# Performance work log

Measured on AMD Instinct MI355X. Metric: run time of the kernel, lower is better.

## Reference

```python
import jax, jax.numpy as jnp
import numpy as np

B, LT, LE, D, H, M, BS = 4, 2048, 1024, 1024, 16, 4096, 128
HD = D // H            # head dim 64
NB = LT // BS          # 16 blocks
SINK_ITERS = 5
NEG = -1e9
SCALE = 1.0 / np.sqrt(HD).astype(np.float32)


def setup_inputs() -> dict:
    key = jax.random.key(0)
    ks = jax.random.split(key, 16)
    p = lambda k, shp: jax.random.normal(k, shp, jnp.float32) * 0.02
    return {
        "targets": jax.random.normal(ks[0], (B, LT, D), jnp.float32),
        "encoded": jax.random.normal(ks[1], (B, LE, D), jnp.float32),
        "ln1_s": jnp.ones((D,), jnp.float32), "ln1_b": jnp.zeros((D,), jnp.float32),
        "ln2_s": jnp.ones((D,), jnp.float32), "ln2_b": jnp.zeros((D,), jnp.float32),
        "ln3_s": jnp.ones((D,), jnp.float32), "ln3_b": jnp.zeros((D,), jnp.float32),
        "wq1": p(ks[2], (D, H, HD)), "wk1": p(ks[3], (D, H, HD)),
        "wv1": p(ks[4], (D, H, HD)), "wo1": p(ks[5], (H, HD, D)),
        "wsort": p(ks[6], (H, HD, NB)),
        "wq2": p(ks[7], (D, H, HD)), "wk2": p(ks[8], (D, H, HD)),
        "wv2": p(ks[9], (D, H, HD)), "wo2": p(ks[10], (H, HD, D)),
        "w1": p(ks[11], (D, M)), "b1": jnp.zeros((M,), jnp.float32),
        "w2": p(ks[12], (M, D)), "b2": jnp.zeros((D,), jnp.float32),
    }


def layer_norm(x, s, b, eps=1e-6):
    mu = jnp.mean(x, -1, keepdims=True)
    var = jnp.mean(jnp.square(x - mu), -1, keepdims=True)
    return (x - mu) * jax.lax.rsqrt(var + eps) * s + b


def causal_sinkhorn(logits):
    # logits: [B,H,NB,NB]. Causal block mask + iterative log-space row/col
    # normalization -> soft (doubly-stochastic-ish) block permutation matrix.
    mask = jnp.tril(jnp.ones((NB, NB), bool))
    la = jnp.where(mask, logits, NEG)
    for _ in range(SINK_ITERS):
        la = la - jax.nn.logsumexp(la, axis=-1, keepdims=True)
        la = jnp.where(mask, la, NEG)
        la = la - jax.nn.logsumexp(la, axis=-2, keepdims=True)
        la = jnp.where(mask, la, NEG)
    return jnp.exp(la)


def sinkhorn_self_attention(x, wq, wk, wv, wsort, wo):
    # x: [B,LT,D] -> blocked q/k/v: [B,NB,BS,H,HD]
    q = jnp.einsum('bld,dhk->blhk', x, wq).reshape(B, NB, BS, H, HD)
    k = jnp.einsum('bld,dhk->blhk', x, wk).reshape(B, NB, BS, H, HD)
    v = jnp.einsum('bld,dhk->blhk', x, wv).reshape(B, NB, BS, H, HD)
    # SortNet: sum-pooled block key representations -> block-to-block logits
    krep = jnp.sum(k, axis=2)                                   # [B,NB,H,HD]
    P = causal_sinkhorn(jnp.einsum('bnhk,hkm->bhnm', krep, wsort))  # [B,H,NB,NB]
    ks = jnp.einsum('bhij,bjshk->bishk', P, k)                  # sorted key blocks
    vs = jnp.einsum('bhij,bjshk->bishk', P, v)
    # each query block attends to (own block [causal]) ++ (sorted block)
    s_loc = jnp.einsum('bnqhk,bnshk->bhnqs', q, k) * SCALE      # [B,H,NB,BS,BS]
    s_srt = jnp.einsum('bnqhk,bnshk->bhnqs', q, ks) * SCALE
    cm = jnp.tril(jnp.ones((BS, BS), bool))
    s_loc = jnp.where(cm, s_loc, NEG)
    w = jax.nn.softmax(jnp.concatenate([s_loc, s_srt], axis=-1), axis=-1)
    o = (jnp.einsum('bhnqs,bnshk->bnqhk', w[..., :BS], v)
         + jnp.einsum('bhnqs,bnshk->bnqhk', w[..., BS:], vs))
    return jnp.einsum('blhk,hkd->bld', o.reshape(B, LT, H, HD), wo)


def cross_attention(x, kv, wq, wk, wv, wo):
    q = jnp.einsum('bld,dhk->blhk', x, wq)
    k = jnp.einsum('bld,dhk->blhk', kv, wk)
    v = jnp.einsum('bld,dhk->blhk', kv, wv)
    w = jax.nn.softmax(jnp.einsum('bqhk,bshk->bhqs', q, k) * SCALE, axis=-1)
    o = jnp.einsum('bhqs,bshk->bqhk', w, v)
    return jnp.einsum('blhk,hkd->bld', o, wo)


def reference(targets, encoded, ln1_s, ln1_b, ln2_s, ln2_b, ln3_s, ln3_b,
              wq1, wk1, wv1, wo1, wsort, wq2, wk2, wv2, wo2, w1, b1, w2, b2):
    x = layer_norm(targets, ln1_s, ln1_b)
    x = sinkhorn_self_attention(x, wq1, wk1, wv1, wsort, wo1) + targets
    y = layer_norm(x, ln2_s, ln2_b)
    y = cross_attention(y, encoded, wq2, wk2, wv2, wo2) + x
    z = layer_norm(y, ln3_s, ln3_b)
    z = jnp.dot(jax.nn.gelu(jnp.dot(z, w1) + b1), w2) + b2
    return y + z
```

## Files before the change

kernel.cpp:

```cpp
#include <hip/hip_runtime.h>

typedef unsigned short u16;
typedef __attribute__((ext_vector_type(8))) short short8;
typedef __attribute__((ext_vector_type(4))) short short4_t;
typedef __attribute__((ext_vector_type(4))) float float4_t;

#define B_ 4
#define LT_ 2048
#define LE_ 1024
#define D_ 1024
#define H_ 16
#define HD_ 64
#define NB_ 16
#define BS_ 128
#define M_ 4096
#define SCALE_ 0.125f

typedef __attribute__((address_space(1))) const void gas_t;
typedef __attribute__((address_space(3))) void las_t;

__device__ __forceinline__ float b2f(u16 u) {
  union { unsigned int i; float f; } v; v.i = ((unsigned int)u) << 16; return v.f;
}
__device__ __forceinline__ u16 f2b(float f) {
  union { float f; unsigned int i; } v; v.f = f;
  unsigned int x = v.i;
  return (u16)((x + 0x7fffu + ((x >> 16) & 1u)) >> 16);
}
__device__ __forceinline__ float gelu_f(float u) {
  float t = 0.7978845608028654f * (u + 0.044715f * u * u * u);
  float th = 1.f - 2.f / (__expf(2.f * t) + 1.f);
  return 0.5f * u * (1.f + th);
}
__device__ __forceinline__ void store_val(u16* p, float x) { *p = f2b(x); }
__device__ __forceinline__ void store_val(float* p, float x) { *p = x; }

__global__ __launch_bounds__(256)
void conv_k(const float* __restrict__ in, u16* __restrict__ out) {
  int i = (blockIdx.x * 256 + threadIdx.x) * 4;
  float4_t v = *(const float4_t*)(in + i);
  short4_t o;
  o[0] = (short)f2b(v[0]); o[1] = (short)f2b(v[1]);
  o[2] = (short)f2b(v[2]); o[3] = (short)f2b(v[3]);
  *(short4_t*)(out + i) = o;
}

__global__ __launch_bounds__(256)
void transpose_k(const float* __restrict__ in, u16* __restrict__ out, int R, int rstride) {
  __shared__ u16 tile[32][33];
  int bx = blockIdx.x * 32, by = blockIdx.y * 32;
  int tx = threadIdx.x & 31, ty = threadIdx.x >> 5;
  #pragma unroll
  for (int y = ty; y < 32; y += 8)
    tile[y][tx] = f2b(in[(size_t)(by + y) * rstride + bx + tx]);
  __syncthreads();
  #pragma unroll
  for (int y = ty; y < 32; y += 8)
    out[(size_t)(bx + y) * R + by + tx] = tile[tx][y];
}

#define NJOBS 10
struct TJobs {
  const float* src[NJOBS];
  u16* dst[NJOBS];
  int outR[NJOBS];
  int inS[NJOBS];
  int ntx[NJOBS];
  int ntiles[NJOBS];
};

__global__ __launch_bounds__(256)
void prep_k(TJobs J) {
  int t = blockIdx.x, j = 0;
  while (t >= J.ntiles[j]) { t -= J.ntiles[j]; ++j; }
  const float* in = J.src[j];
  u16* out = J.dst[j];
  const int R = J.outR[j], rstride = J.inS[j];
  const int bx = (t % J.ntx[j]) * 32, by = (t / J.ntx[j]) * 32;
  __shared__ u16 tile[32][33];
  int tx = threadIdx.x & 31, ty = threadIdx.x >> 5;
  #pragma unroll
  for (int y = ty; y < 32; y += 8)
    tile[y][tx] = f2b(in[(size_t)(by + y) * rstride + bx + tx]);
  __syncthreads();
  #pragma unroll
  for (int y = ty; y < 32; y += 8)
    out[(size_t)(bx + y) * R + by + tx] = tile[tx][y];
}

__global__ __launch_bounds__(256)
void ln_k(const float* __restrict__ x, const float* __restrict__ sw,
          const float* __restrict__ bw, u16* __restrict__ out) {
  int row = blockIdx.x, tid = threadIdx.x;
  const float* xr = x + (size_t)row * 1024 + tid * 4;
  float4_t raw = *(const float4_t*)xr;
  float v0 = raw[0], v1 = raw[1], v2 = raw[2], v3 = raw[3];
  float sum = v0 + v1 + v2 + v3;
  #pragma unroll
  for (int off = 32; off > 0; off >>= 1) sum += __shfl_down(sum, off, 64);
  __shared__ float sA[4], sB[4];
  int w = tid >> 6;
  if ((tid & 63) == 0) sA[w] = sum;
  __syncthreads();
  float mu = (sA[0] + sA[1] + sA[2] + sA[3]) * (1.f / 1024.f);
  float d0 = v0 - mu, d1 = v1 - mu, d2 = v2 - mu, d3 = v3 - mu;
  float s2 = d0 * d0 + d1 * d1 + d2 * d2 + d3 * d3;
  #pragma unroll
  for (int off = 32; off > 0; off >>= 1) s2 += __shfl_down(s2, off, 64);
  if ((tid & 63) == 0) sB[w] = s2;
  __syncthreads();
  float inv = rsqrtf((sB[0] + sB[1] + sB[2] + sB[3]) * (1.f / 1024.f) + 1e-6f);
  float4_t sv = *(const float4_t*)(sw + tid * 4);
  float4_t bv = *(const float4_t*)(bw + tid * 4);
  short4_t ov;
  ov[0] = (short)f2b(d0 * inv * sv[0] + bv[0]);
  ov[1] = (short)f2b(d1 * inv * sv[1] + bv[1]);
  ov[2] = (short)f2b(d2 * inv * sv[2] + bv[2]);
  ov[3] = (short)f2b(d3 * inv * sv[3] + bv[3]);
  *(short4_t*)(out + (size_t)row * 1024 + tid * 4) = ov;
}

template<int EPI, typename TC, int SPLIT>
__global__ __launch_bounds__(256)
void gemm_k(const u16* __restrict__ A, const u16* __restrict__ Bt,
            const float* __restrict__ bias, const float* __restrict__ res,
            TC* __restrict__ C, int M, int N, int K, size_t cstride) {
  __shared__ __align__(16) u16 lA[128 * 32];
  __shared__ __align__(16) u16 lB[128 * 32];
  const int gx = gridDim.x;
  int lin = blockIdx.y * gx + blockIdx.x;
  const int nwg = gx * gridDim.y;
  if (!(nwg & 7)) {
    const int chunk = nwg >> 3;
    lin = (lin & 7) * chunk + (lin >> 3);
  }
  const int bn = (lin % gx) * 128;
  const int bm = (lin / gx) * 128;
  const int tid = threadIdx.x;
  const int lane = tid & 63;
  const int wave = tid >> 6;
  const int wy = wave >> 1, wx = wave & 1;
  const int quad = lane >> 4, l16 = lane & 15;

  float4_t acc[4][4];
  float4_t zz = {0.f, 0.f, 0.f, 0.f};
  #pragma unroll
  for (int i = 0; i < 4; ++i)
    #pragma unroll
    for (int j = 0; j < 4; ++j) acc[i][j] = zz;

  const int r0 = tid >> 2, kc0 = (tid & 3) * 8;
  const u16* gA0 = A + (size_t)(bm + r0) * K + kc0;
  const u16* gA1 = A + (size_t)(bm + 64 + r0) * K + kc0;
  const u16* gB0 = Bt + (size_t)(bn + r0) * K + kc0;
  const u16* gB1 = Bt + (size_t)(bn + 64 + r0) * K + kc0;
  u16* lA0 = &lA[tid * 8];
  u16* lA1 = &lA[(tid + 256) * 8];
  u16* lB0 = &lB[tid * 8];
  u16* lB1 = &lB[(tid + 256) * 8];

  for (int k0 = 0; k0 < K; k0 += 32) {
    __syncthreads();
    __builtin_amdgcn_global_load_lds((gas_t*)(gA0 + k0), (las_t*)lA0, 16, 0, 0);
    __builtin_amdgcn_global_load_lds((gas_t*)(gA1 + k0), (las_t*)lA1, 16, 0, 0);
    __builtin_amdgcn_global_load_lds((gas_t*)(gB0 + k0), (las_t*)lB0, 16, 0, 0);
    __builtin_amdgcn_global_load_lds((gas_t*)(gB1 + k0), (las_t*)lB1, 16, 0, 0);
    __syncthreads();
    short8 af[4], bfr[4];
    #pragma unroll
    for (int i = 0; i < 4; ++i)
      af[i] = *(const short8*)&lA[(wy * 64 + i * 16 + l16) * 32 + quad * 8];
    #pragma unroll
    for (int j = 0; j < 4; ++j)
      bfr[j] = *(const short8*)&lB[(wx * 64 + j * 16 + l16) * 32 + quad * 8];
    #pragma unroll
    for (int i = 0; i < 4; ++i)
      #pragma unroll
      for (int j = 0; j < 4; ++j)
        acc[i][j] = __builtin_amdgcn_mfma_f32_16x16x32_bf16(af[i], bfr[j], acc[i][j], 0, 0, 0);
  }

  #pragma unroll
  for (int i = 0; i < 4; ++i) {
    int row = bm + wy * 64 + i * 16 + quad * 4;
    #pragma unroll
    for (int j = 0; j < 4; ++j) {
      int col = bn + wx * 64 + j * 16 + l16;
      TC* Cb = SPLIT ? (C + (size_t)(col >> 10) * cstride) : C;
      int ccol = SPLIT ? (col & 1023) : col;
      int cn = SPLIT ? 1024 : N;
      #pragma unroll
      for (int v = 0; v < 4; ++v) {
        float x = acc[i][j][v];
        size_t idx = (size_t)(row + v) * cn + ccol;
        if (EPI == 1) {
          x += res[idx];
        } else if (EPI == 2) {
          x = gelu_f(x + bias[col]);
        } else if (EPI == 3) {
          x += bias[col] + res[idx];
        }
        store_val(&Cb[idx], x);
      }
    }
  }
}

template<int EPI, typename TC, int SPLIT>
__global__ __launch_bounds__(512, 2)
void gemm256_k(const u16* __restrict__ A, const u16* __restrict__ Bt,
               const float* __restrict__ bias, const float* __restrict__ res,
               TC* __restrict__ C, int M, int N, int K, size_t cstride) {
  __shared__ __align__(16) u16 lA[4][256 * 32];
  __shared__ __align__(16) u16 lB[4][256 * 32];
  const int gx = gridDim.x;
  int lin = blockIdx.y * gx + blockIdx.x;
  const int nwg = gx * gridDim.y;
  if (!(nwg & 7)) {
    const int chunk = nwg >> 3;
    lin = (lin & 7) * chunk + (lin >> 3);
  }
  const int bn = (lin % gx) * 256;
  const int bm = (lin / gx) * 256;
  const int tid = threadIdx.x;
  const int lane = tid & 63;
  const int wave = tid >> 6;
  const int wy = wave >> 2, wx = wave & 3;
  const int quad = lane >> 4, l16 = lane & 15;
  const int slo = ((quad ^ ((l16 >> 1) & 3)) << 4);

  int lrow[2], kcs[2];
  #pragma unroll
  for (int u = 0; u < 2; ++u) {
    int p = (tid + u * 512) * 16;
    int lg = p ^ (((p >> 7) & 3) << 4);
    lrow[u] = lg >> 6;
    kcs[u] = (lg & 63) >> 1;
  }
  const u16* gA[2]; const u16* gB[2];
  #pragma unroll
  for (int u = 0; u < 2; ++u) {
    gA[u] = A + (size_t)(bm + lrow[u]) * K + kcs[u];
    gB[u] = Bt + (size_t)(bn + lrow[u]) * K + kcs[u];
  }
  const int NT = K >> 5;

  float4_t acc[8][4];
  float4_t zz = {0.f, 0.f, 0.f, 0.f};
  #pragma unroll
  for (int i = 0; i < 8; ++i)
    #pragma unroll
    for (int j = 0; j < 4; ++j) acc[i][j] = zz;

  #define STAGE256(TT, BUF)                                                      \
    {                                                                            \
      int kk_ = (TT) * 32;                                                       \
      __builtin_amdgcn_global_load_lds((gas_t*)(gA[0] + kk_),                    \
          (las_t*)((char*)&lA[BUF][0] + tid * 16), 16, 0, 0);                    \
      __builtin_amdgcn_global_load_lds((gas_t*)(gA[1] + kk_),                    \
          (las_t*)((char*)&lA[BUF][0] + (tid + 512) * 16), 16, 0, 0);            \
      __builtin_amdgcn_global_load_lds((gas_t*)(gB[0] + kk_),                    \
          (las_t*)((char*)&lB[BUF][0] + tid * 16), 16, 0, 0);                    \
      __builtin_amdgcn_global_load_lds((gas_t*)(gB[1] + kk_),                    \
          (las_t*)((char*)&lB[BUF][0] + (tid + 512) * 16), 16, 0, 0);            \
    }

  STAGE256(0, 0)
  STAGE256(1, 1)
  STAGE256(2, 2)

  for (int t = 0; t < NT; ++t) {
    asm volatile("s_waitcnt vmcnt(8)" ::: "memory");
    __builtin_amdgcn_s_barrier();
    __builtin_amdgcn_sched_barrier(0);
    int ts = t + 3; if (ts > NT - 1) ts = NT - 1;
    STAGE256(ts, (t + 3) & 3)
    const char* bufA = (const char*)&lA[t & 3][0];
    const char* bufB = (const char*)&lB[t & 3][0];
    short8 af[8], bf[4];
    #pragma unroll
    for (int i = 0; i < 8; ++i)
      af[i] = *(const short8*)(bufA + (wy * 128 + i * 16 + l16) * 64 + slo);
    #pragma unroll
    for (int j = 0; j < 4; ++j)
      bf[j] = *(const short8*)(bufB + (wx * 64 + j * 16 + l16) * 64 + slo);
    __builtin_amdgcn_s_setprio(1);
    #pragma unroll
    for (int i = 0; i < 8; ++i)
      #pragma unroll
      for (int j = 0; j < 4; ++j)
        acc[i][j] = __builtin_amdgcn_mfma_f32_16x16x32_bf16(af[i], bf[j], acc[i][j], 0, 0, 0);
    __builtin_amdgcn_s_setprio(0);
  }
  #undef STAGE256

  #pragma unroll
  for (int i = 0; i < 8; ++i) {
    int row = bm + wy * 128 + i * 16 + quad * 4;
    #pragma unroll
    for (int j = 0; j < 4; ++j) {
      int col = bn + wx * 64 + j * 16 + l16;
      TC* Cb = SPLIT ? (C + (size_t)(col >> 10) * cstride) : C;
      int ccol = SPLIT ? (col & 1023) : col;
      int cn = SPLIT ? 1024 : N;
      #pragma unroll
      for (int v = 0; v < 4; ++v) {
        float x = acc[i][j][v];
        size_t idx = (size_t)(row + v) * cn + ccol;
        if (EPI == 1) {
          x += res[idx];
        } else if (EPI == 2) {
          x = gelu_f(x + bias[col]);
        } else if (EPI == 3) {
          x += bias[col] + res[idx];
        }
        store_val(&Cb[idx], x);
      }
    }
  }
}

__global__ __launch_bounds__(256)
void krep_k(const u16* __restrict__ K1, float* __restrict__ krep) {
  int idx = blockIdx.x * 256 + threadIdx.x;
  int col = idx & 1023;
  int bn = idx >> 10;
  const u16* p = K1 + (size_t)bn * 128 * 1024 + col;
  float s = 0.f;
  for (int i = 0; i < 128; ++i) s += b2f(p[(size_t)i * 1024]);
  krep[idx] = s;
}

__global__ __launch_bounds__(256)
void sinkhorn_k(const float* __restrict__ krep, const float* __restrict__ wsort,
                float* __restrict__ P) {
  int bh = blockIdx.x;
  int b = bh >> 4, h = bh & 15;
  int t = threadIdx.x;
  int i = t >> 4, j = t & 15;
  __shared__ float la[16][17];
  __shared__ float red[16];
  float acc = 0.f;
  const float* kr = krep + ((size_t)b * 16 + i) * 1024 + h * 64;
  const float* ws = wsort + (size_t)h * 64 * 16 + j;
  for (int k = 0; k < 64; ++k) acc += kr[k] * ws[k * 16];
  la[i][j] = (j <= i) ? acc : -1e9f;
  __syncthreads();
  for (int it = 0; it < 5; ++it) {
    if (t < 16) {
      float m = -1e30f;
      for (int jj = 0; jj < 16; ++jj) m = fmaxf(m, la[t][jj]);
      float s = 0.f;
      for (int jj = 0; jj < 16; ++jj) s += __expf(la[t][jj] - m);
      red[t] = m + __logf(s);
    }
    __syncthreads();
    la[i][j] = (j <= i) ? la[i][j] - red[i] : -1e9f;
    __syncthreads();
    if (t < 16) {
      float m = -1e30f;
      for (int ii = 0; ii < 16; ++ii) m = fmaxf(m, la[ii][t]);
      float s = 0.f;
      for (int ii = 0; ii < 16; ++ii) s += __expf(la[ii][t] - m);
      red[t] = m + __logf(s);
    }
    __syncthreads();
    la[i][j] = (j <= i) ? la[i][j] - red[j] : -1e9f;
    __syncthreads();
  }
  P[((size_t)bh * 16 + i) * 16 + j] = __expf(la[i][j]);
}

__global__ __launch_bounds__(256)
void sortmix_k(const float* __restrict__ P, const u16* __restrict__ K1,
               const u16* __restrict__ V1, u16* __restrict__ KS,
               u16* __restrict__ VS) {
  int t = blockIdx.x * 256 + threadIdx.x;
  int col = (t & 127) * 8;
  int rest = t >> 7;
  int b = rest >> 11, is = rest & 2047, i = is >> 7, s = is & 127;
  int h = col >> 6;
  const float* Pr = P + (((size_t)(b * 16 + h)) * 16 + i) * 16;
  size_t base = ((size_t)(b * 2048 + s)) * 1024 + col;
  float ka[8] = {0, 0, 0, 0, 0, 0, 0, 0}, va[8] = {0, 0, 0, 0, 0, 0, 0, 0};
  for (int j = 0; j <= i; ++j) {
    float p = Pr[j];
    short8 kk = *(const short8*)&K1[base + (size_t)j * 131072];
    short8 vv = *(const short8*)&V1[base + (size_t)j * 131072];
    #pragma unroll
    for (int e = 0; e < 8; ++e) {
      ka[e] += p * b2f((u16)kk[e]);
      va[e] += p * b2f((u16)vv[e]);
    }
  }
  size_t ob = ((size_t)(b * 2048 + i * 128 + s)) * 1024 + col;
  short8 ok, ov;
  #pragma unroll
  for (int e = 0; e < 8; ++e) { ok[e] = (short)f2b(ka[e]); ov[e] = (short)f2b(va[e]); }
  *(short8*)&KS[ob] = ok;
  *(short8*)&VS[ob] = ov;
}

#define KLS 72
#define VTS 136
#define PLS 136

template<int CROSS>
__global__ __launch_bounds__(256)
void attn_mfma_k(const u16* __restrict__ Q, const u16* __restrict__ Ka,
                 const u16* __restrict__ Va, const u16* __restrict__ Kb2,
                 const u16* __restrict__ Vb2, u16* __restrict__ O) {
  __shared__ __align__(16) u16 kls[128 * KLS];
  __shared__ __align__(16) u16 vtls[64 * VTS];
  __shared__ __align__(16) u16 pls[128 * PLS];
  const int blk = blockIdx.x;
  const int n = blk & 15, h = (blk >> 4) & 15, b = blk >> 8;
  const int tid = threadIdx.x, lane = tid & 63, wv = tid >> 6;
  const int quad = lane >> 4, l16 = lane & 15;
  const int m0 = wv * 32;
  const size_t qrowbase = (size_t)b * 2048 + n * 128;

  short8 qa[2][2];
  #pragma unroll
  for (int qi = 0; qi < 2; ++qi)
    #pragma unroll
    for (int ks = 0; ks < 2; ++ks)
      qa[qi][ks] = *(const short8*)&Q[(qrowbase + m0 + qi * 16 + l16) * 1024 +
                                      h * 64 + ks * 32 + quad * 8];

  float4_t acc_o[2][4];
  float mrow[2], lrow[2];
  #pragma unroll
  for (int mi = 0; mi < 2; ++mi) {
    #pragma unroll
    for (int dn = 0; dn < 4; ++dn) acc_o[mi][dn] = {0.f, 0.f, 0.f, 0.f};
    mrow[mi] = -1e30f; lrow[mi] = 0.f;
  }

  const int NT = CROSS ? 8 : 2;
  for (int t = 0; t < NT; ++t) {
    const u16 *Kg, *Vg;
    bool causal = false;
    if (CROSS) {
      size_t kb = ((size_t)b * 1024 + t * 128) * 1024 + h * 64;
      Kg = Ka + kb; Vg = Va + kb;
    } else if (t == 0) {
      size_t kb = qrowbase * 1024 + h * 64;
      Kg = Ka + kb; Vg = Va + kb; causal = true;
    } else {
      size_t kb = qrowbase * 1024 + h * 64;
      Kg = Kb2 + kb; Vg = Vb2 + kb;
    }
    __syncthreads();
    #pragma unroll
    for (int i = 0; i < 4; ++i) {
      int c = tid + i * 256;
      int row = c >> 3, dd = (c & 7) * 8;
      short8 kv = *(const short8*)&Kg[(size_t)row * 1024 + dd];
      *(short8*)&kls[row * KLS + dd] = kv;
      short8 vv = *(const short8*)&Vg[(size_t)row * 1024 + dd];
      #pragma unroll
      for (int e = 0; e < 8; ++e) vtls[(dd + e) * VTS + row] = (u16)vv[e];
    }
    __syncthreads();

    float4_t s[2][8];
    #pragma unroll
    for (int qi = 0; qi < 2; ++qi)
      #pragma unroll
      for (int nj = 0; nj < 8; ++nj) s[qi][nj] = {0.f, 0.f, 0.f, 0.f};
    #pragma unroll
    for (int nj = 0; nj < 8; ++nj) {
      short8 k0 = *(const short8*)&kls[(nj * 16 + l16) * KLS + quad * 8];
      short8 k1 = *(const short8*)&kls[(nj * 16 + l16) * KLS + 32 + quad * 8];
      #pragma unroll
      for (int qi = 0; qi < 2; ++qi) {
        s[qi][nj] = __builtin_amdgcn_mfma_f32_16x16x32_bf16(k0, qa[qi][0], s[qi][nj], 0, 0, 0);
        s[qi][nj] = __builtin_amdgcn_mfma_f32_16x16x32_bf16(k1, qa[qi][1], s[qi][nj], 0, 0, 0);
      }
    }

    float crv[2];
    #pragma unroll
    for (int qi = 0; qi < 2; ++qi) {
      const int qrow = m0 + qi * 16 + l16;
      float mx = -1e30f;
      #pragma unroll
      for (int nj = 0; nj < 8; ++nj)
        #pragma unroll
        for (int v = 0; v < 4; ++v) {
          float x = s[qi][nj][v] * SCALE_;
          if (causal && (nj * 16 + quad * 4 + v > qrow)) x = -1e30f;
          s[qi][nj][v] = x;
          mx = fmaxf(mx, x);
        }
      mx = fmaxf(mx, __shfl_xor(mx, 16, 64));
      mx = fmaxf(mx, __shfl_xor(mx, 32, 64));
      float mn = fmaxf(mrow[qi], mx);
      crv[qi] = __expf(mrow[qi] - mn);
      mrow[qi] = mn;
      float rs = 0.f;
      #pragma unroll
      for (int nj = 0; nj < 8; ++nj)
        #pragma unroll
        for (int v = 0; v < 4; ++v) {
          float p = __expf(s[qi][nj][v] - mn);
          s[qi][nj][v] = p;
          rs += p;
        }
      rs += __shfl_xor(rs, 16, 64);
      rs += __shfl_xor(rs, 32, 64);
      lrow[qi] = lrow[qi] * crv[qi] + rs;
      #pragma unroll
      for (int nj = 0; nj < 8; ++nj) {
        unsigned p01 = (unsigned)f2b(s[qi][nj][0]) | ((unsigned)f2b(s[qi][nj][1]) << 16);
        unsigned p23 = (unsigned)f2b(s[qi][nj][2]) | ((unsigned)f2b(s[qi][nj][3]) << 16);
        *(unsigned*)&pls[qrow * PLS + nj * 16 + quad * 4] = p01;
        *(unsigned*)&pls[qrow * PLS + nj * 16 + quad * 4 + 2] = p23;
      }
    }
    #pragma unroll
    for (int mi = 0; mi < 2; ++mi)
      #pragma unroll
      for (int v = 0; v < 4; ++v) {
        float c = __shfl(crv[mi], quad * 20 + v, 64);
        #pragma unroll
        for (int dn = 0; dn < 4; ++dn) acc_o[mi][dn][v] *= c;
      }

    #pragma unroll
    for (int ks = 0; ks < 4; ++ks) {
      short8 a0 = *(const short8*)&pls[(m0 + l16) * PLS + ks * 32 + quad * 8];
      short8 a1 = *(const short8*)&pls[(m0 + 16 + l16) * PLS + ks * 32 + quad * 8];
      #pragma unroll
      for (int dn = 0; dn < 4; ++dn) {
        short8 bv = *(const short8*)&vtls[(dn * 16 + l16) * VTS + ks * 32 + quad * 8];
        acc_o[0][dn] = __builtin_amdgcn_mfma_f32_16x16x32_bf16(a0, bv, acc_o[0][dn], 0, 0, 0);
        acc_o[1][dn] = __builtin_amdgcn_mfma_f32_16x16x32_bf16(a1, bv, acc_o[1][dn], 0, 0, 0);
      }
    }
  }
  #pragma unroll
  for (int mi = 0; mi < 2; ++mi) {
    float invl = 1.f / lrow[mi];
    #pragma unroll
    for (int v = 0; v < 4; ++v) {
      float inv = __shfl(invl, quad * 20 + v, 64);
      int rowl = m0 + mi * 16 + quad * 4 + v;
      #pragma unroll
      for (int dn = 0; dn < 4; ++dn)
        O[(qrowbase + rowl) * 1024 + h * 64 + dn * 16 + l16] =
            f2b(acc_o[mi][dn][v] * inv);
    }
  }
}

extern "C" void kernel_launch(void* const* d_in, const int* in_sizes, int n_in,
                              void* d_out, int out_size, void* d_ws, size_t ws_size,
                              hipStream_t stream) {
  const float* targets = (const float*)d_in[0];
  const float* encoded = (const float*)d_in[1];
  const float* ln1s = (const float*)d_in[2];
  const float* ln1b = (const float*)d_in[3];
  const float* ln2s = (const float*)d_in[4];
  const float* ln2b = (const float*)d_in[5];
  const float* ln3s = (const float*)d_in[6];
  const float* ln3b = (const float*)d_in[7];
  const float* wq1 = (const float*)d_in[8];
  const float* wk1 = (const float*)d_in[9];
  const float* wv1 = (const float*)d_in[10];
  const float* wo1 = (const float*)d_in[11];
  const float* wsort = (const float*)d_in[12];
  const float* wq2 = (const float*)d_in[13];
  const float* wk2 = (const float*)d_in[14];
  const float* wv2 = (const float*)d_in[15];
  const float* wo2 = (const float*)d_in[16];
  const float* w1 = (const float*)d_in[17];
  const float* b1 = (const float*)d_in[18];
  const float* w2 = (const float*)d_in[19];
  const float* b2 = (const float*)d_in[20];
  float* out = (float*)d_out;
  (void)in_sizes; (void)n_in; (void)out_size;

  char* ws = (char*)d_ws;
  size_t off = 0;
  auto alloc = [&](size_t n) -> char* {
    char* p = ws + off;
    off += (n + 255) & ~(size_t)255;
    return p;
  };

  const size_t NTD = (size_t)B_ * LT_ * D_;
  const size_t NEED_BIG = (size_t)(8 * 2 + 8 + 8) * 1024 * 1024
                        + (size_t)LE_ * B_ * D_ * 2
                        + NTD * 2 * 7
                        + (1u << 20);

  if (ws_size >= NEED_BIG) {
    u16* wq1t = (u16*)alloc((size_t)1024 * 1024 * 2);
    u16* wk1t = (u16*)alloc((size_t)1024 * 1024 * 2);
    u16* wv1t = (u16*)alloc((size_t)1024 * 1024 * 2);
    u16* wo1t = (u16*)alloc((size_t)1024 * 1024 * 2);
    u16* wq2t = (u16*)alloc((size_t)1024 * 1024 * 2);
    u16* wk2t = (u16*)alloc((size_t)1024 * 1024 * 2);
    u16* wv2t = (u16*)alloc((size_t)1024 * 1024 * 2);
    u16* wo2t = (u16*)alloc((size_t)1024 * 1024 * 2);
    u16* w1t = (u16*)alloc((size_t)4096 * 1024 * 2);
    u16* w2t = (u16*)alloc((size_t)1024 * 4096 * 2);
    u16* Eb  = (u16*)alloc((size_t)B_ * LE_ * D_ * 2);
    u16* XLN = (u16*)alloc(NTD * 2);
    u16* Qb  = (u16*)alloc(NTD * 2);
    u16* Kb  = (u16*)alloc(NTD * 2);
    u16* Vb  = (u16*)alloc(NTD * 2);
    u16* KSb = (u16*)alloc(NTD * 2);
    u16* VSb = (u16*)alloc(NTD * 2);
    u16* Ob  = (u16*)alloc(NTD * 2);
    float* KREP = (float*)alloc((size_t)B_ * NB_ * 1024 * 4);
    float* Pm = (float*)alloc((size_t)B_ * H_ * NB_ * NB_ * 4);
    u16* HML = Qb;

    TJobs J;
    const float* srcs[NJOBS] = {wq1, wk1, wv1, wo1, wq2, wk2, wv2, wo2, w1, w2};
    u16* dsts[NJOBS] = {wq1t, wk1t, wv1t, wo1t, wq2t, wk2t, wv2t, wo2t, w1t, w2t};
    int total = 0;
    for (int j = 0; j < NJOBS; ++j) {
      J.src[j] = srcs[j]; J.dst[j] = dsts[j];
      if (j < 8)      { J.outR[j] = 1024; J.inS[j] = 1024; J.ntx[j] = 32;  J.ntiles[j] = 1024; }
      else if (j == 8){ J.outR[j] = 1024; J.inS[j] = 4096; J.ntx[j] = 128; J.ntiles[j] = 4096; }
      else            { J.outR[j] = 4096; J.inS[j] = 1024; J.ntx[j] = 32;  J.ntiles[j] = 4096; }
      total += J.ntiles[j];
    }
    prep_k<<<total, 256, 0, stream>>>(J);
    conv_k<<<4096, 256, 0, stream>>>(encoded, Eb);

    ln_k<<<8192, 256, 0, stream>>>(targets, ln1s, ln1b, XLN);
    gemm256_k<0, u16, 1><<<dim3(12, 32), 512, 0, stream>>>(XLN, wq1t, nullptr, nullptr,
                                                           Qb, 8192, 3072, 1024, NTD);
    krep_k<<<256, 256, 0, stream>>>(Kb, KREP);
    sinkhorn_k<<<64, 256, 0, stream>>>(KREP, wsort, Pm);
    sortmix_k<<<4096, 256, 0, stream>>>(Pm, Kb, Vb, KSb, VSb);
    attn_mfma_k<0><<<1024, 256, 0, stream>>>(Qb, Kb, Vb, KSb, VSb, Ob);
    gemm_k<1, float, 0><<<dim3(8, 64), 256, 0, stream>>>(Ob, wo1t, nullptr, targets, out, 8192, 1024, 1024, 0);
    ln_k<<<8192, 256, 0, stream>>>(out, ln2s, ln2b, XLN);
    gemm_k<0, u16, 0><<<dim3(8, 64), 256, 0, stream>>>(XLN, wq2t, nullptr, nullptr, Qb, 8192, 1024, 1024, 0);
    gemm_k<0, u16, 1><<<dim3(16, 32), 256, 0, stream>>>(Eb, wk2t, nullptr, nullptr, Kb, 4096, 2048, 1024, NTD);
    attn_mfma_k<1><<<1024, 256, 0, stream>>>(Qb, Kb, Vb, nullptr, nullptr, Ob);
    gemm_k<1, float, 0><<<dim3(8, 64), 256, 0, stream>>>(Ob, wo2t, nullptr, out, out, 8192, 1024, 1024, 0);
    ln_k<<<8192, 256, 0, stream>>>(out, ln3s, ln3b, XLN);
    gemm256_k<2, u16, 0><<<dim3(16, 32), 512, 0, stream>>>(XLN, w1t, b1, nullptr, HML, 8192, 4096, 1024, 0);
    gemm_k<3, float, 0><<<dim3(8, 64), 256, 0, stream>>>(HML, w2t, b2, out, out, 8192, 1024, 4096, 0);
    return;
  }

  const size_t SLC = (size_t)LT_ * D_;
  u16* wT  = (u16*)alloc((size_t)1024 * 1024 * 2);
  u16* XLN = (u16*)alloc(SLC * 2);
  u16* Qb  = (u16*)alloc(SLC * 2);
  u16* Kb  = (u16*)alloc(SLC * 2);
  u16* Vb  = (u16*)alloc(SLC * 2);
  u16* KSb = (u16*)alloc(SLC * 2);
  u16* VSb = (u16*)alloc(SLC * 2);
  u16* Ob  = (u16*)alloc(SLC * 2);
  u16* Hc  = (u16*)alloc(SLC * 2);
  u16* Eb  = (u16*)alloc((size_t)LE_ * D_ * 2);
  float* KREP = (float*)alloc((size_t)NB_ * 1024 * 4);
  float* Pm = (float*)alloc((size_t)H_ * NB_ * NB_ * 4);

  auto T = [&](const float* src, int rs) {
    transpose_k<<<dim3(32, 32), 256, 0, stream>>>(src, wT, 1024, rs);
  };

  for (int b = 0; b < B_; ++b) {
    const float* tgt_b = targets + (size_t)b * SLC;
    const float* enc_b = encoded + (size_t)b * LE_ * D_;
    float* out_b = out + (size_t)b * SLC;

    ln_k<<<2048, 256, 0, stream>>>(tgt_b, ln1s, ln1b, XLN);
    T(wq1, 1024);
    gemm_k<0, u16, 0><<<dim3(8, 16), 256, 0, stream>>>(XLN, wT, nullptr, nullptr, Qb, 2048, 1024, 1024, 0);
    T(wk1, 1024);
    gemm_k<0, u16, 0><<<dim3(8, 16), 256, 0, stream>>>(XLN, wT, nullptr, nullptr, Kb, 2048, 1024, 1024, 0);
    T(wv1, 1024);
    gemm_k<0, u16, 0><<<dim3(8, 16), 256, 0, stream>>>(XLN, wT, nullptr, nullptr, Vb, 2048, 1024, 1024, 0);
    krep_k<<<64, 256, 0, stream>>>(Kb, KREP);
    sinkhorn_k<<<16, 256, 0, stream>>>(KREP, wsort, Pm);
    sortmix_k<<<1024, 256, 0, stream>>>(Pm, Kb, Vb, KSb, VSb);
    attn_mfma_k<0><<<256, 256, 0, stream>>>(Qb, Kb, Vb, KSb, VSb, Ob);
    T(wo1, 1024);
    gemm_k<1, float, 0><<<dim3(8, 16), 256, 0, stream>>>(Ob, wT, nullptr, tgt_b, out_b, 2048, 1024, 1024, 0);
    ln_k<<<2048, 256, 0, stream>>>(out_b, ln2s, ln2b, XLN);
    conv_k<<<1024, 256, 0, stream>>>(enc_b, Eb);
    T(wq2, 1024);
    gemm_k<0, u16, 0><<<dim3(8, 16), 256, 0, stream>>>(XLN, wT, nullptr, nullptr, Qb, 2048, 1024, 1024, 0);
    T(wk2, 1024);
    gemm_k<0, u16, 0><<<dim3(8, 8), 256, 0, stream>>>(Eb, wT, nullptr, nullptr, Kb, 1024, 1024, 1024, 0);
    T(wv2, 1024);
    gemm_k<0, u16, 0><<<dim3(8, 8), 256, 0, stream>>>(Eb, wT, nullptr, nullptr, Vb, 1024, 1024, 1024, 0);
    attn_mfma_k<1><<<256, 256, 0, stream>>>(Qb, Kb, Vb, nullptr, nullptr, Ob);
    T(wo2, 1024);
    gemm_k<1, float, 0><<<dim3(8, 16), 256, 0, stream>>>(Ob, wT, nullptr, out_b, out_b, 2048, 1024, 1024, 0);
    ln_k<<<2048, 256, 0, stream>>>(out_b, ln3s, ln3b, XLN);
    for (int c = 0; c < 4; ++c) {
      T(w1 + (size_t)c * 1024, 4096);
      gemm_k<2, u16, 0><<<dim3(8, 16), 256, 0, stream>>>(XLN, wT, b1 + c * 1024, nullptr, Hc,
                                                         2048, 1024, 1024, 0);
      T(w2 + (size_t)c * 1024 * 1024, 1024);
      if (c < 3)
        gemm_k<1, float, 0><<<dim3(8, 16), 256, 0, stream>>>(Hc, wT, nullptr, out_b, out_b,
                                                             2048, 1024, 1024, 0);
      else
        gemm_k<3, float, 0><<<dim3(8, 16), 256, 0, stream>>>(Hc, wT, b2, out_b, out_b,
                                                             2048, 1024, 1024, 0);
    }
  }
}
```

Measured before the change: 794.3 us.

## Swizzle attention LDS tiles, pass P via shuffles, remap workgroups across XCDs

Replaces the padded LDS layouts in the MFMA attention kernel with XOR-swizzled unpadded tiles for K and the transposed V. V is now staged linearly in LDS and transposed in a second LDS pass, instead of scalar scattered stores. The softmax probabilities stay in registers and are redistributed into MFMA A-operand layout with cross-lane shuffles, which removes the P tile from LDS. Block indices are also remapped in chunks of eight, apparently to group related workgroups on the same XCD for cache locality. The trade-offs are many extra shuffles, an added LDS round trip for V, and a reworked barrier placement.

```diff
diff --git a/kernel.cpp b/kernel.cpp
--- a/kernel.cpp
+++ b/kernel.cpp
@@ -1,6 +1,7 @@
 #include <hip/hip_runtime.h>
 
 typedef unsigned short u16;
+typedef unsigned int u32;
 typedef __attribute__((ext_vector_type(8))) short short8;
 typedef __attribute__((ext_vector_type(4))) short short4_t;
 typedef __attribute__((ext_vector_type(4))) float float4_t;
@@ -401,19 +402,19 @@
   *(short8*)&VS[ob] = ov;
 }
 
-#define KLS 72
-#define VTS 136
-#define PLS 136
-
 template<int CROSS>
 __global__ __launch_bounds__(256)
 void attn_mfma_k(const u16* __restrict__ Q, const u16* __restrict__ Ka,
                  const u16* __restrict__ Va, const u16* __restrict__ Kb2,
                  const u16* __restrict__ Vb2, u16* __restrict__ O) {
-  __shared__ __align__(16) u16 kls[128 * KLS];
-  __shared__ __align__(16) u16 vtls[64 * VTS];
-  __shared__ __align__(16) u16 pls[128 * PLS];
-  const int blk = blockIdx.x;
+  __shared__ __align__(16) u16 kls[128 * 64];
+  __shared__ __align__(16) u16 vlin[128 * 64];
+  __shared__ __align__(16) u16 vtls[64 * 128];
+  int blk = blockIdx.x;
+  {
+    int nwg = gridDim.x;
+    if (!(nwg & 7)) { int ch = nwg >> 3; blk = (blk & 7) * ch + (blk >> 3); }
+  }
   const int n = blk & 15, h = (blk >> 4) & 15, b = blk >> 8;
   const int tid = threadIdx.x, lane = tid & 63, wv = tid >> 6;
   const int quad = lane >> 4, l16 = lane & 15;
@@ -451,19 +452,29 @@
       size_t kb = qrowbase * 1024 + h * 64;
       Kg = Kb2 + kb; Vg = Vb2 + kb;
     }
-    __syncthreads();
     #pragma unroll
     for (int i = 0; i < 4; ++i) {
       int c = tid + i * 256;
-      int row = c >> 3, dd = (c & 7) * 8;
-      short8 kv = *(const short8*)&Kg[(size_t)row * 1024 + dd];
-      *(short8*)&kls[row * KLS + dd] = kv;
-      short8 vv = *(const short8*)&Vg[(size_t)row * 1024 + dd];
-      #pragma unroll
-      for (int e = 0; e < 8; ++e) vtls[(dd + e) * VTS + row] = (u16)vv[e];
+      int row = c >> 3, slot = c & 7, dd = slot * 8;
+      short8 kv8 = *(const short8*)&Kg[(size_t)row * 1024 + dd];
+      *(short8*)&kls[row * 64 + ((slot ^ (row & 7)) * 8)] = kv8;
+      short8 vv8 = *(const short8*)&Vg[(size_t)row * 1024 + dd];
+      *(short8*)&vlin[row * 64 + dd] = vv8;
     }
     __syncthreads();
 
+    #pragma unroll
+    for (int ii = 0; ii < 4; ++ii) {
+      int d = tid & 63;
+      int kvg = (tid >> 6) * 4 + ii;
+      union { short8 s8; u16 us[8]; } tt;
+      #pragma unroll
+      for (int j = 0; j < 8; ++j)
+        tt.us[j] = vlin[(kvg * 8 + j) * 64 + d];
+      int slotp = (kvg & 8) | ((kvg ^ (d & 7)) & 7);
+      *(short8*)&vtls[d * 128 + slotp * 8] = tt.s8;
+    }
+
     float4_t s[2][8];
     #pragma unroll
     for (int qi = 0; qi < 2; ++qi)
@@ -471,8 +482,9 @@
       for (int nj = 0; nj < 8; ++nj) s[qi][nj] = {0.f, 0.f, 0.f, 0.f};
     #pragma unroll
     for (int nj = 0; nj < 8; ++nj) {
-      short8 k0 = *(const short8*)&kls[(nj * 16 + l16) * KLS + quad * 8];
-      short8 k1 = *(const short8*)&kls[(nj * 16 + l16) * KLS + 32 + quad * 8];
+      int r = nj * 16 + l16;
+      short8 k0 = *(const short8*)&kls[r * 64 + ((quad ^ (l16 & 7)) * 8)];
+      short8 k1 = *(const short8*)&kls[r * 64 + (((4 + quad) ^ (l16 & 7)) * 8)];
       #pragma unroll
       for (int qi = 0; qi < 2; ++qi) {
         s[qi][nj] = __builtin_amdgcn_mfma_f32_16x16x32_bf16(k0, qa[qi][0], s[qi][nj], 0, 0, 0);
@@ -481,6 +493,7 @@
     }
 
     float crv[2];
+    u32 p01[2][8], p23[2][8];
     #pragma unroll
     for (int qi = 0; qi < 2; ++qi) {
       const int qrow = m0 + qi * 16 + l16;
@@ -513,10 +526,8 @@
       lrow[qi] = lrow[qi] * crv[qi] + rs;
       #pragma unroll
       for (int nj = 0; nj < 8; ++nj) {
-        unsigned p01 = (unsigned)f2b(s[qi][nj][0]) | ((unsigned)f2b(s[qi][nj][1]) << 16);
-        unsigned p23 = (unsigned)f2b(s[qi][nj][2]) | ((unsigned)f2b(s[qi][nj][3]) << 16);
-        *(unsigned*)&pls[qrow * PLS + nj * 16 + quad * 4] = p01;
-        *(unsigned*)&pls[qrow * PLS + nj * 16 + quad * 4 + 2] = p23;
+        p01[qi][nj] = (u32)f2b(s[qi][nj][0]) | ((u32)f2b(s[qi][nj][1]) << 16);
+        p23[qi][nj] = (u32)f2b(s[qi][nj][2]) | ((u32)f2b(s[qi][nj][3]) << 16);
       }
     }
     #pragma unroll
@@ -528,15 +539,37 @@
         for (int dn = 0; dn < 4; ++dn) acc_o[mi][dn][v] *= c;
       }
 
+    __syncthreads();
+
+    const int src0 = (quad & 1) * 32 + l16;
+    const int src1 = src0 + 16;
+    const bool hi = (quad >> 1) != 0;
     #pragma unroll
     for (int ks = 0; ks < 4; ++ks) {
-      short8 a0 = *(const short8*)&pls[(m0 + l16) * PLS + ks * 32 + quad * 8];
-      short8 a1 = *(const short8*)&pls[(m0 + 16 + l16) * PLS + ks * 32 + quad * 8];
+      union { short8 s8; u32 u[4]; } au[2];
+      #pragma unroll
+      for (int qi = 0; qi < 2; ++qi) {
+        u32 w0a = __shfl(p01[qi][2 * ks],     src0, 64);
+        u32 w0b = __shfl(p01[qi][2 * ks + 1], src0, 64);
+        u32 w1a = __shfl(p23[qi][2 * ks],     src0, 64);
+        u32 w1b = __shfl(p23[qi][2 * ks + 1], src0, 64);
+        u32 w2a = __shfl(p01[qi][2 * ks],     src1, 64);
+        u32 w2b = __shfl(p01[qi][2 * ks + 1], src1, 64);
+        u32 w3a = __shfl(p23[qi][2 * ks],     src1, 64);
+        u32 w3b = __shfl(p23[qi][2 * ks + 1], src1, 64);
+        au[qi].u[0] = hi ? w0b : w0a;
+        au[qi].u[1] = hi ? w1b : w1a;
+        au[qi].u[2] = hi ? w2b : w2a;
+        au[qi].u[3] = hi ? w3b : w3a;
+      }
       #pragma unroll
       for (int dn = 0; dn < 4; ++dn) {
-        short8 bv = *(const short8*)&vtls[(dn * 16 + l16) * VTS + ks * 32 + quad * 8];
-        acc_o[0][dn] = __builtin_amdgcn_mfma_f32_16x16x32_bf16(a0, bv, acc_o[0][dn], 0, 0, 0);
-        acc_o[1][dn] = __builtin_amdgcn_mfma_f32_16x16x32_bf16(a1, bv, acc_o[1][dn], 0, 0, 0);
+        int dR = dn * 16 + l16;
+        int sbase = ks * 4 + quad;
+        int sp = (sbase & 8) | ((sbase ^ (l16 & 7)) & 7);
+        short8 bv = *(const short8*)&vtls[dR * 128 + sp * 8];
+        acc_o[0][dn] = __builtin_amdgcn_mfma_f32_16x16x32_bf16(au[0].s8, bv, acc_o[0][dn], 0, 0, 0);
+        acc_o[1][dn] = __builtin_amdgcn_mfma_f32_16x16x32_bf16(au[1].s8, bv, acc_o[1][dn], 0, 0, 0);
       }
     }
   }
```

Result: slower. 860.5 us (+8.3%).
